# Kernel optimization log

Hardware: AMD Instinct MI355X
Metric: run time of the kernel (lower is better)

## Reference

```python
import jax, jax.numpy as jnp
import numpy as np

FEATURE_DIM = 512
NUM_LABEL = 128
NUM_HEADS = 8
K = 8192
THRES = 0.95


def enqueue(queue, keys, count):
    """FIFO enqueue: queue[count:] = queue[:K-count]; queue[:count] = keys[:count].
    queue: [K, d] (transpose of torch layout), keys: [B, d], count: traced int scalar."""
    Kq = queue.shape[0]
    idx = jnp.arange(Kq)
    shifted = jnp.take(queue, jnp.clip(idx - count, 0, Kq - 1), axis=0)
    new_keys = jnp.take(keys, jnp.clip(idx, 0, keys.shape[0] - 1), axis=0)
    return jnp.where((idx < count)[:, None], new_keys, shifted)


def masked_enqueue(queue, keys, mask):
    # torch boolean indexing keeps original order -> stable sort selected to front
    order = jnp.argsort(~mask, stable=True)
    return enqueue(queue, jnp.take(keys, order, axis=0), jnp.sum(mask))


def forward_cross(x, mem_k, mem_v, Wq, Wk, Wo, bo):
    """Multi-head cross-attention: queries x [N,d], keys mem_k [K,d], values mem_v [K,L].
    Per-head scores on feature_dim; value (label) dim not head-split (L % heads != 0 in
    general), heads averaged; output projection L->L."""
    N, d = x.shape
    dh = d // NUM_HEADS
    q = (x @ Wq).reshape(N, NUM_HEADS, dh)
    k = (mem_k @ Wk).reshape(-1, NUM_HEADS, dh)
    scores = jnp.einsum('nhd,khd->hnk', q, k) * (dh ** -0.5)  # [H,N,K]
    attn = jax.nn.softmax(scores, axis=-1).mean(axis=0)       # [N,K]
    return attn @ mem_v @ Wo + bo                             # [N,L]


def setup_inputs() -> dict:
    key = jax.random.key(0)
    ks = jax.random.split(key, 16)
    N, B_LB = 4096, 1024

    def norm_rows(a):
        return a / jnp.linalg.norm(a, axis=1, keepdims=True)

    inp = {
        'anchor_feat': jax.random.normal(ks[0], (N, FEATURE_DIM), jnp.float32),
        'positive_feat': jax.random.normal(ks[1], (N, FEATURE_DIM), jnp.float32),
        'lb_feat': jax.random.normal(ks[2], (B_LB, FEATURE_DIM), jnp.float32),
        'lb_one_hot': jax.random.uniform(ks[3], (B_LB, NUM_LABEL), jnp.float32),
        'logits_x_lb': jax.random.uniform(ks[4], (B_LB, NUM_LABEL), jnp.float32),
        'logits_x_ulb_1': jax.random.uniform(ks[5], (N, NUM_LABEL), jnp.float32),
        'logits_x_ulb_2': jax.random.uniform(ks[6], (N, NUM_LABEL), jnp.float32),
        # queue buffers: stored [K, d] (= torch queue.T); feat queues L2-normalized at init
        'feat_queue1': norm_rows(jax.random.normal(ks[7], (K, FEATURE_DIM), jnp.float32)),
        'feat_queue2': norm_rows(jax.random.normal(ks[8], (K, FEATURE_DIM), jnp.float32)),
        'label_queue1': norm_rows(jax.random.normal(ks[9], (K, NUM_LABEL), jnp.float32)),
        'label_queue2': norm_rows(jax.random.normal(ks[10], (K, NUM_LABEL), jnp.float32)),
        # Block (cross-attention) parameters
        'Wq': jax.random.normal(ks[11], (FEATURE_DIM, FEATURE_DIM), jnp.float32) * (FEATURE_DIM ** -0.5),
        'Wk': jax.random.normal(ks[12], (FEATURE_DIM, FEATURE_DIM), jnp.float32) * (FEATURE_DIM ** -0.5),
        'Wo': jax.random.normal(ks[13], (NUM_LABEL, NUM_LABEL), jnp.float32) * (NUM_LABEL ** -0.5),
        'bo': jnp.zeros((NUM_LABEL,), jnp.float32),
    }
    return inp


def reference(anchor_feat, positive_feat, lb_feat, lb_one_hot, logits_x_lb,
              logits_x_ulb_1, logits_x_ulb_2,
              feat_queue1, feat_queue2, label_queue1, label_queue2,
              Wq, Wk, Wo, bo):
    sg = jax.lax.stop_gradient  # enqueue is @torch.no_grad()
    B = lb_feat.shape[0] // 2
    lb_feat_1, lb_feat_2 = sg(lb_feat[:B]), sg(lb_feat[B:])
    lb_oh_1, lb_oh_2 = sg(lb_one_hot[:B]), sg(lb_one_hot[B:])

    # queue 1: labeled chunk 1, then high-confidence anchors
    fq1 = enqueue(feat_queue1, lb_feat_1, B)
    lq1 = enqueue(label_queue1, lb_oh_1, B)
    ulb_1_max = jnp.max(logits_x_ulb_1, axis=1) > THRES
    fq1 = masked_enqueue(fq1, sg(anchor_feat), ulb_1_max)
    lq1 = masked_enqueue(lq1, sg(logits_x_ulb_1), ulb_1_max)

    # queue 2: labeled chunk 2, then high-confidence positives
    fq2 = enqueue(feat_queue2, lb_feat_2, B)
    lq2 = enqueue(label_queue2, lb_oh_2, B)
    ulb_2_max = jnp.max(logits_x_ulb_2, axis=1) > THRES
    fq2 = masked_enqueue(fq2, sg(positive_feat), ulb_2_max)
    lq2 = masked_enqueue(lq2, sg(logits_x_ulb_2), ulb_2_max)

    out1 = forward_cross(anchor_feat, fq1, lq1, Wq, Wk, Wo, bo)
    out2 = forward_cross(positive_feat, fq2, lq2, Wq, Wk, Wo, bo)
    # stacked new ulb logits (other original outputs are identity passthroughs)
    return jnp.stack([out1, out2], axis=0)
```

## Files before the change

### kernel.cpp

```cpp
#include <hip/hip_runtime.h>

typedef __bf16 bf16;
typedef __bf16 bf16x8 __attribute__((ext_vector_type(8)));
typedef float f32x4 __attribute__((ext_vector_type(4)));

#define MFMA16(a,b,c) __builtin_amdgcn_mfma_f32_16x16x32_bf16(a,b,c,0,0,0)

#if __has_builtin(__builtin_amdgcn_exp2f)
#define EXP2(x) __builtin_amdgcn_exp2f(x)
#else
#define EXP2(x) exp2f(x)
#endif

#define GLOAD16(g, l) __builtin_amdgcn_global_load_lds( \
    (const __attribute__((address_space(1))) void*)(g), \
    (__attribute__((address_space(3))) void*)(l), 16, 0, 0)

#define N_Q   4096
#define DFEAT 512
#define KQ    8192
#define NLAB  128
#define NHEAD 8
#define KVB   32

#define MBv (1024ull*1024ull)
#define OFF_COUNTS 0ull
#define OFF_MODE   512ull
#define OFF_FLAGS  1024ull
#define OFF_SEL    (64ull*1024ull)
#define OFF_FQ1    (1ull*MBv)
#define OFF_FQ2    (9ull*MBv)
#define OFF_LQ1    (17ull*MBv)
#define OFF_LQ2    (19ull*MBv)
#define OFF_Q1     (21ull*MBv)
#define OFF_Q2     (25ull*MBv)
#define OFF_K1     (29ull*MBv)
#define OFF_WQT    (45ull*MBv)
#define OFF_WKT    (46ull*MBv)
#define OFF_WOT    (47ull*MBv)
#define OFF_VWT    (48ull*MBv)
#define OFF_ACC    (52ull*MBv)

__device__ __forceinline__ float loads(const void* p, size_t i, int f32m) {
    return f32m ? ((const float*)p)[i] : (float)((const bf16*)p)[i];
}
__device__ __forceinline__ bf16x8 load8(const void* p, size_t i, int f32m) {
    bf16x8 r;
    if (f32m) {
        const float4* q = (const float4*)((const float*)p + i);
        float4 f0 = q[0], f1 = q[1];
        r[0] = (bf16)f0.x; r[1] = (bf16)f0.y; r[2] = (bf16)f0.z; r[3] = (bf16)f0.w;
        r[4] = (bf16)f1.x; r[5] = (bf16)f1.y; r[6] = (bf16)f1.z; r[7] = (bf16)f1.w;
    } else {
        r = *(const bf16x8*)((const bf16*)p + i);
    }
    return r;
}

__global__ void detect_kernel(const void* probe, int* mode) {
    const unsigned short* u = (const unsigned short*)probe;
    int t = threadIdx.x;
    int bad = 0;
    for (int i = t; i < 2048; i += 256) {
        unsigned short v = u[2 * i];
        int e = (v >> 7) & 0xFF;
        if (e > 140 || (e < 60 && e != 0)) bad++;
    }
    __shared__ int sb[256];
    sb[t] = bad;
    __syncthreads();
    for (int off = 128; off; off >>= 1) {
        if (t < off) sb[t] += sb[t + off];
        __syncthreads();
    }
    if (t == 0) mode[0] = (sb[0] > 200) ? 1 : 0;
}

__global__ void flag_kernel(const void* __restrict__ ulb1, const void* __restrict__ ulb2,
                            int* __restrict__ flags, const int* __restrict__ modep) {
    int f32m = *modep;
    int row = blockIdx.x, s = blockIdx.y, t = threadIdx.x;
    const void* p = s ? ulb2 : ulb1;
    size_t base = (size_t)row * NLAB;
    float m = fmaxf(loads(p, base + t, f32m), loads(p, base + t + 64, f32m));
    #pragma unroll
    for (int off = 32; off; off >>= 1) m = fmaxf(m, __shfl_xor(m, off));
    if (t == 0) flags[s * N_Q + row] = (m > 0.95f) ? 1 : 0;
}

__global__ void scan_kernel(const int* __restrict__ flags, int* __restrict__ sel,
                            int* __restrict__ counts) {
    int s = blockIdx.x, t = threadIdx.x;
    const int* f = flags + s * N_Q;
    int* selp = sel + s * N_Q;
    __shared__ int ls[1024];
    int f0 = f[t*4], f1 = f[t*4+1], f2 = f[t*4+2], f3 = f[t*4+3];
    int local = f0 + f1 + f2 + f3;
    ls[t] = local;
    __syncthreads();
    for (int off = 1; off < 1024; off <<= 1) {
        int v = (t >= off) ? ls[t - off] : 0;
        __syncthreads();
        ls[t] += v;
        __syncthreads();
    }
    int pos = ls[t] - local;
    if (f0) selp[pos++] = t*4;
    if (f1) selp[pos++] = t*4+1;
    if (f2) selp[pos++] = t*4+2;
    if (f3) selp[pos++] = t*4+3;
    if (t == 1023) counts[s] = ls[1023];
}

__global__ void buildq_kernel(const void* __restrict__ anchor, const void* __restrict__ positive,
                              const void* __restrict__ lbfeat, const void* __restrict__ lboh,
                              const void* __restrict__ ulb1, const void* __restrict__ ulb2,
                              const void* __restrict__ fq1i, const void* __restrict__ fq2i,
                              const void* __restrict__ lq1i, const void* __restrict__ lq2i,
                              const int* __restrict__ sel, const int* __restrict__ counts,
                              bf16* __restrict__ fq1o, bf16* __restrict__ fq2o,
                              bf16* __restrict__ lq1o, bf16* __restrict__ lq2o,
                              const int* __restrict__ modep) {
    int f32m = *modep;
    int i = blockIdx.x, s = blockIdx.y, t = threadIdx.x;
    int C = counts[s];
    const void *fb, *lb;
    size_t frow, lrow;
    if (i < C) {
        int r = sel[s * N_Q + i];
        fb = s ? positive : anchor; frow = r;
        lb = s ? ulb2 : ulb1;       lrow = r;
    } else if (i < C + 512) {
        int r = i - C + s * 512;
        fb = lbfeat; frow = r;
        lb = lboh;   lrow = r;
    } else {
        int r = i - C - 512;
        fb = s ? fq2i : fq1i; frow = r;
        lb = s ? lq2i : lq1i; lrow = r;
    }
    bf16* fd = (s ? fq2o : fq1o) + (size_t)i * DFEAT;
    bf16* ld = (s ? lq2o : lq1o) + (size_t)i * NLAB;
    if (t < 64)      *(bf16x8*)&fd[t * 8]        = load8(fb, frow * DFEAT + (size_t)t * 8, f32m);
    else if (t < 80) *(bf16x8*)&ld[(t - 64) * 8] = load8(lb, lrow * NLAB + (size_t)(t - 64) * 8, f32m);
}

__global__ void transpose_kernel(const void* __restrict__ W, bf16* __restrict__ T, int n,
                                 const int* __restrict__ modep) {
    int f32m = *modep;
    __shared__ bf16 tile[32][33];
    int bx = blockIdx.x * 32, by = blockIdx.y * 32;
    int tx = threadIdx.x & 31, ty = threadIdx.x >> 5;
    for (int r = ty; r < 32; r += 8) tile[r][tx] = (bf16)loads(W, (size_t)(by + r) * n + bx + tx, f32m);
    __syncthreads();
    for (int r = ty; r < 32; r += 8) T[(size_t)(bx + r) * n + by + tx] = tile[tx][r];
}

__launch_bounds__(256, 2)
__global__ void gemm_nt(const void* __restrict__ A, const void* __restrict__ A2,
                        const bf16* __restrict__ B,
                        bf16* __restrict__ C, bf16* __restrict__ C2,
                        int M, int N, int Kd, float alpha,
                        const int* __restrict__ modep, int a_raw, int swz) {
    int f32m = a_raw ? *modep : 0;
    if (blockIdx.z) { A = A2; C = C2; }
    __shared__ __align__(16) bf16 As[128 * 72];
    __shared__ __align__(16) bf16 Bs[128 * 72];
    int m0 = blockIdx.x * 128, n0 = blockIdx.y * 128;
    int t = threadIdx.x, lane = t & 63, wid = t >> 6;
    int quad = lane >> 4, l15 = lane & 15;
    int wrow = (wid >> 1) * 64, wcol = (wid & 1) * 64;
    int srow = t >> 1, sseg = t & 1;
    f32x4 acc[4][4] = {};
    for (int k0 = 0; k0 < Kd; k0 += 32) {
        __syncthreads();
        bf16x8 a0 = load8(A, (size_t)(m0 + srow) * Kd + k0 + sseg * 8, f32m);
        bf16x8 a1 = load8(A, (size_t)(m0 + srow) * Kd + k0 + (sseg + 2) * 8, f32m);
        const uint4* gb = (const uint4*)(B + (size_t)(n0 + srow) * Kd + k0);
        uint4 b0 = gb[sseg], b1 = gb[sseg + 2];
        *(bf16x8*)&As[srow * 72 + sseg * 8]       = a0;
        *(bf16x8*)&As[srow * 72 + (sseg + 2) * 8] = a1;
        *(uint4*)&Bs[srow * 72 + sseg * 8]        = b0;
        *(uint4*)&Bs[srow * 72 + (sseg + 2) * 8]  = b1;
        __syncthreads();
        bf16x8 af[4], bfr[4];
        #pragma unroll
        for (int mt = 0; mt < 4; mt++) af[mt]  = *(const bf16x8*)&As[(wrow + mt*16 + l15) * 72 + quad * 8];
        #pragma unroll
        for (int nt = 0; nt < 4; nt++) bfr[nt] = *(const bf16x8*)&Bs[(wcol + nt*16 + l15) * 72 + quad * 8];
        #pragma unroll
        for (int mt = 0; mt < 4; mt++)
            #pragma unroll
            for (int nt = 0; nt < 4; nt++)
                acc[mt][nt] = MFMA16(af[mt], bfr[nt], acc[mt][nt]);
    }
    #pragma unroll
    for (int mt = 0; mt < 4; mt++)
        #pragma unroll
        for (int nt = 0; nt < 4; nt++)
            #pragma unroll
            for (int r = 0; r < 4; r++) {
                int row = m0 + wrow + mt*16 + quad*4 + r;
                int col = n0 + wcol + nt*16 + l15;
                if (swz) col = (col & ~31) | (((col & 12) << 1) | ((col & 16) >> 2) | (col & 3));
                C[(size_t)row * N + col] = (bf16)(acc[mt][nt][r] * alpha);
            }
}

__launch_bounds__(256, 2)
__global__ void flash3_kernel(const bf16* __restrict__ q1, const bf16* __restrict__ q2,
                              const bf16* __restrict__ kbase, const bf16* __restrict__ vbase,
                              float* __restrict__ acc_out) {
    __shared__ __align__(16) char smem[49152];
    int qb = blockIdx.x, h = blockIdx.y, s = blockIdx.z;
    const bf16* Q  = s ? q2 : q1;
    const bf16* Kp = kbase + (size_t)s * KQ * DFEAT + h * 64;
    const bf16* Vp = vbase + (size_t)s * KQ;
    int t = threadIdx.x, lane = t & 63, wid = t >> 6;
    int quad = lane >> 4, l15 = lane & 15;
    int wq = wid & 1, wh = wid >> 1;
    int qbase = qb * 128 + wq * 64;

    bf16x8 qf[4][2];
    #pragma unroll
    for (int mt = 0; mt < 4; mt++)
        #pragma unroll
        for (int ch = 0; ch < 2; ch++)
            qf[mt][ch] = *(const bf16x8*)(Q + (size_t)(qbase + mt*16 + l15) * DFEAT + h*64 + ch*32 + quad*8);

    bf16x8 onesf;
    #pragma unroll
    for (int i = 0; i < 8; i++) onesf[i] = (bf16)1.0f;

    bf16* Kt = (bf16*)smem;
    bf16* Vt = (bf16*)(smem + 16384);

    int srow8 = lane >> 3;
    int sslot = (lane & 7) ^ srow8;
    const bf16* KgH = Kp + (size_t)(wh * 4096) * DFEAT + (size_t)srow8 * DFEAT + sslot * 8;
    const bf16* VgH = Vp + wh * 4096 + (size_t)(2*srow8 + (sslot >> 2)) * (2 * KQ) + (sslot & 3) * 8;

    const int h7 = l15 & 7;
    int kro[2][2], vro[8];
    #pragma unroll
    for (int nt = 0; nt < 2; nt++)
        #pragma unroll
        for (int ch = 0; ch < 2; ch++)
            kro[nt][ch] = (nt*16 + l15) * 64 + (((ch*4 + quad) ^ h7) << 3);
    #pragma unroll
    for (int ct = 0; ct < 8; ct++)
        vro[ct] = (ct*8 + (l15 >> 1)) * 64 + (((((l15 & 1) << 2) | quad) ^ (l15 >> 1)) << 3);

    {
        bf16* kb = Kt + (size_t)(wh*2 + 0) * 2048;
        bf16* vb = Vt + (size_t)(wh*2 + 0) * 4096;
        if (wq == 0) {
            #pragma unroll
            for (int c = 0; c < 4; c++) GLOAD16(KgH + (size_t)c*8*DFEAT, kb + c*512);
            #pragma unroll
            for (int c = 0; c < 2; c++) GLOAD16(VgH + (size_t)c*16*(2*KQ), vb + c*512);
        } else {
            #pragma unroll
            for (int c = 2; c < 8; c++) GLOAD16(VgH + (size_t)c*16*(2*KQ), vb + c*512);
        }
    }
    __syncthreads();

    f32x4 O[4][8] = {};
    f32x4 L[4] = {};

    for (int it = 0; it < 4096 / KVB; it++) {
        int p = it & 1;
        if (it + 1 < 4096 / KVB) {
            int kvn = (it + 1) * KVB;
            bf16* kb = Kt + (size_t)(wh*2 + (p^1)) * 2048;
            bf16* vb = Vt + (size_t)(wh*2 + (p^1)) * 4096;
            if (wq == 0) {
                #pragma unroll
                for (int c = 0; c < 4; c++) GLOAD16(KgH + (size_t)kvn*DFEAT + (size_t)c*8*DFEAT, kb + c*512);
                #pragma unroll
                for (int c = 0; c < 2; c++) GLOAD16(VgH + kvn + (size_t)c*16*(2*KQ), vb + c*512);
            } else {
                #pragma unroll
                for (int c = 2; c < 8; c++) GLOAD16(VgH + kvn + (size_t)c*16*(2*KQ), vb + c*512);
            }
        }
        const bf16* Kb = Kt + (size_t)(wh*2 + p) * 2048;
        const bf16* Vb = Vt + (size_t)(wh*2 + p) * 4096;

        bf16x8 kf[2][2];
        #pragma unroll
        for (int nt = 0; nt < 2; nt++)
            #pragma unroll
            for (int ch = 0; ch < 2; ch++)
                kf[nt][ch] = *(const bf16x8*)&Kb[kro[nt][ch]];

        bf16x8 P[4];
        __builtin_amdgcn_s_setprio(1);
        #pragma unroll
        for (int mt = 0; mt < 4; mt++) {
            f32x4 s0 = {}, s1 = {};
            s0 = MFMA16(kf[0][0], qf[mt][0], s0);
            s0 = MFMA16(kf[0][1], qf[mt][1], s0);
            s1 = MFMA16(kf[1][0], qf[mt][0], s1);
            s1 = MFMA16(kf[1][1], qf[mt][1], s1);
            bf16x8 pp;
            #pragma unroll
            for (int r = 0; r < 4; r++) {
                pp[r]     = (bf16)EXP2(s0[r]);
                pp[4 + r] = (bf16)EXP2(s1[r]);
            }
            P[mt] = pp;
        }
        #pragma unroll
        for (int mt = 0; mt < 4; mt++) L[mt] = MFMA16(P[mt], onesf, L[mt]);
        #pragma unroll
        for (int ct = 0; ct < 8; ct++) {
            bf16x8 vf = *(const bf16x8*)&Vb[vro[ct]];
            #pragma unroll
            for (int mt = 0; mt < 4; mt++)
                O[mt][ct] = MFMA16(P[mt], vf, O[mt][ct]);
        }
        __builtin_amdgcn_s_setprio(0);
        __syncthreads();
    }

    f32x4* MP = (f32x4*)smem;
    int midx = lane * 36;
    #pragma unroll
    for (int pass = 0; pass < 2; pass++) {
        if (wh == 1 && wq == pass) {
            #pragma unroll
            for (int mt = 0; mt < 4; mt++) {
                #pragma unroll
                for (int ct = 0; ct < 8; ct++) MP[midx + mt*8 + ct] = O[mt][ct];
                MP[midx + 32 + mt] = L[mt];
            }
        }
        __syncthreads();
        if (wh == 0 && wq == pass) {
            #pragma unroll
            for (int mt = 0; mt < 4; mt++) {
                f32x4 lp = MP[midx + 32 + mt];
                float invr[4];
                #pragma unroll
                for (int r = 0; r < 4; r++) invr[r] = 1.0f / (8.0f * (L[mt][r] + lp[r]));
                #pragma unroll
                for (int ct = 0; ct < 8; ct++) {
                    f32x4 op = MP[midx + mt*8 + ct];
                    #pragma unroll
                    for (int r = 0; r < 4; r++) {
                        int row = qbase + mt*16 + quad*4 + r;
                        atomicAdd(&acc_out[((size_t)s * N_Q + row) * NLAB + ct*16 + l15],
                                  (O[mt][ct][r] + op[r]) * invr[r]);
                    }
                }
            }
        }
        __syncthreads();
    }
}

__global__ void bias_kernel(const float* __restrict__ acc, const void* __restrict__ bo,
                            void* __restrict__ out, const int* __restrict__ modep) {
    int f32m = *modep;
    int idx = blockIdx.x * 256 + threadIdx.x;
    float v = acc[idx] + loads(bo, idx & (NLAB - 1), f32m);
    if (f32m) ((float*)out)[idx] = v;
    else      ((bf16*)out)[idx] = (bf16)v;
}

extern "C" void kernel_launch(void* const* d_in, const int* in_sizes, int n_in,
                              void* d_out, int out_size, void* d_ws, size_t ws_size,
                              hipStream_t stream) {
    const void* anchor   = d_in[0];
    const void* positive = d_in[1];
    const void* lbfeat   = d_in[2];
    const void* lboh     = d_in[3];
    const void* ulb1     = d_in[5];
    const void* ulb2     = d_in[6];
    const void* fq1i     = d_in[7];
    const void* fq2i     = d_in[8];
    const void* lq1i     = d_in[9];
    const void* lq2i     = d_in[10];
    const void* Wq       = d_in[11];
    const void* Wk       = d_in[12];
    const void* Wo       = d_in[13];
    const void* bo       = d_in[14];

    char* ws = (char*)d_ws;
    int*  counts = (int*)(ws + OFF_COUNTS);
    int*  modep  = (int*)(ws + OFF_MODE);
    int*  flags  = (int*)(ws + OFF_FLAGS);
    int*  sel    = (int*)(ws + OFF_SEL);
    bf16* fq1  = (bf16*)(ws + OFF_FQ1);
    bf16* fq2  = (bf16*)(ws + OFF_FQ2);
    bf16* lq1  = (bf16*)(ws + OFF_LQ1);
    bf16* lq2  = (bf16*)(ws + OFF_LQ2);
    bf16* q1   = (bf16*)(ws + OFF_Q1);
    bf16* q2   = (bf16*)(ws + OFF_Q2);
    bf16* k1   = (bf16*)(ws + OFF_K1);
    bf16* wqT  = (bf16*)(ws + OFF_WQT);
    bf16* wkT  = (bf16*)(ws + OFF_WKT);
    bf16* woT  = (bf16*)(ws + OFF_WOT);
    bf16* vwt  = (bf16*)(ws + OFF_VWT);
    float* accb = (float*)(ws + OFF_ACC);

    hipMemsetAsync(accb, 0, (size_t)2 * N_Q * NLAB * sizeof(float), stream);

    detect_kernel<<<1, 256, 0, stream>>>(anchor, modep);
    flag_kernel<<<dim3(N_Q, 2), 64, 0, stream>>>(ulb1, ulb2, flags, modep);
    scan_kernel<<<2, 1024, 0, stream>>>(flags, sel, counts);
    buildq_kernel<<<dim3(KQ, 2), 128, 0, stream>>>(anchor, positive, lbfeat, lboh, ulb1, ulb2,
                                                   fq1i, fq2i, lq1i, lq2i, sel, counts,
                                                   fq1, fq2, lq1, lq2, modep);
    transpose_kernel<<<dim3(16, 16), 256, 0, stream>>>(Wq, wqT, 512, modep);
    transpose_kernel<<<dim3(16, 16), 256, 0, stream>>>(Wk, wkT, 512, modep);
    transpose_kernel<<<dim3(4, 4), 256, 0, stream>>>(Wo, woT, 128, modep);

    const float qalpha = 0.125f * 1.44269504088896f;
    gemm_nt<<<dim3(32, 4, 2), 256, 0, stream>>>(anchor, positive, wqT, q1, q2,
                                                4096, 512, 512, qalpha, modep, 1, 0);
    gemm_nt<<<dim3(128, 4, 1), 256, 0, stream>>>(fq1, nullptr, wkT, k1, nullptr,
                                                 16384, 512, 512, 1.0f, modep, 0, 0);
    gemm_nt<<<dim3(1, 128, 1), 256, 0, stream>>>(woT, nullptr, lq1, vwt, nullptr,
                                                 128, 16384, 128, 1.0f, modep, 0, 0);

    flash3_kernel<<<dim3(32, NHEAD, 2), 256, 0, stream>>>(q1, q2, k1, vwt, accb);
    bias_kernel<<<(2 * N_Q * NLAB) / 256, 256, 0, stream>>>(accb, bo, d_out, modep);
}
```

Measured before the change: 372.1 us.

## Merge setup and projection kernels into fewer launches with inline dtype probe

Replaces the separate detect, flag and three transpose kernels with one prep kernel, and the three projection GEMM launches with a single gemm3 kernel dispatched by block index. Each kernel now works out the input dtype itself from a small probe of the anchor tensor, so there is no longer a mode word in the workspace to read. This cuts the launch count and the serial dependency gaps between small kernels. The smaller probe sample (32 values instead of 2048) could misclassify the dtype on unusual inputs.

```diff
diff --git a/kernel.cpp b/kernel.cpp
--- a/kernel.cpp
+++ b/kernel.cpp
@@ -25,7 +25,6 @@
 
 #define MBv (1024ull*1024ull)
 #define OFF_COUNTS 0ull
-#define OFF_MODE   512ull
 #define OFF_FLAGS  1024ull
 #define OFF_SEL    (64ull*1024ull)
 #define OFF_FQ1    (1ull*MBv)
@@ -41,6 +40,18 @@
 #define OFF_VWT    (48ull*MBv)
 #define OFF_ACC    (52ull*MBv)
 
+__device__ __forceinline__ int probe_f32(const void* p) {
+    const unsigned short* u = (const unsigned short*)p;
+    int bad = 0;
+    #pragma unroll
+    for (int i = 0; i < 32; i++) {
+        unsigned short v = u[2 * i];
+        int e = (v >> 7) & 0xFF;
+        if (e > 140 || (e < 60 && e != 0)) bad++;
+    }
+    return bad > 3;
+}
+
 __device__ __forceinline__ float loads(const void* p, size_t i, int f32m) {
     return f32m ? ((const float*)p)[i] : (float)((const bf16*)p)[i];
 }
@@ -57,35 +68,43 @@
     return r;
 }
 
-__global__ void detect_kernel(const void* probe, int* mode) {
-    const unsigned short* u = (const unsigned short*)probe;
-    int t = threadIdx.x;
-    int bad = 0;
-    for (int i = t; i < 2048; i += 256) {
-        unsigned short v = u[2 * i];
-        int e = (v >> 7) & 0xFF;
-        if (e > 140 || (e < 60 && e != 0)) bad++;
-    }
-    __shared__ int sb[256];
-    sb[t] = bad;
+__device__ __forceinline__ void do_transpose(const void* W, bf16* T, int n,
+                                             int bxi, int byi, int f32m, bf16 (*tile)[33]) {
+    int bx = bxi * 32, by = byi * 32;
+    int tx = threadIdx.x & 31, ty = threadIdx.x >> 5;
+    for (int r = ty; r < 32; r += 8) tile[r][tx] = (bf16)loads(W, (size_t)(by + r) * n + bx + tx, f32m);
     __syncthreads();
-    for (int off = 128; off; off >>= 1) {
-        if (t < off) sb[t] += sb[t + off];
-        __syncthreads();
-    }
-    if (t == 0) mode[0] = (sb[0] > 200) ? 1 : 0;
-}
-
-__global__ void flag_kernel(const void* __restrict__ ulb1, const void* __restrict__ ulb2,
-                            int* __restrict__ flags, const int* __restrict__ modep) {
-    int f32m = *modep;
-    int row = blockIdx.x, s = blockIdx.y, t = threadIdx.x;
-    const void* p = s ? ulb2 : ulb1;
-    size_t base = (size_t)row * NLAB;
-    float m = fmaxf(loads(p, base + t, f32m), loads(p, base + t + 64, f32m));
-    #pragma unroll
-    for (int off = 32; off; off >>= 1) m = fmaxf(m, __shfl_xor(m, off));
-    if (t == 0) flags[s * N_Q + row] = (m > 0.95f) ? 1 : 0;
+    for (int r = ty; r < 32; r += 8) T[(size_t)(bx + r) * n + by + tx] = tile[tx][r];
+}
+
+__global__ void prep_kernel(const void* __restrict__ Wq, const void* __restrict__ Wk,
+                            const void* __restrict__ Wo,
+                            bf16* __restrict__ wqT, bf16* __restrict__ wkT, bf16* __restrict__ woT,
+                            const void* __restrict__ ulb1, const void* __restrict__ ulb2,
+                            int* __restrict__ flags, const void* __restrict__ probe) {
+    __shared__ bf16 tile[32][33];
+    int f32m = probe_f32(probe);
+    int b = blockIdx.x, t = threadIdx.x;
+    if (b < 2048) {
+        int idx = b * 4 + (t >> 6);
+        int lane = t & 63;
+        int s = idx >> 12, row = idx & 4095;
+        const void* p = s ? ulb2 : ulb1;
+        size_t base = (size_t)row * NLAB;
+        float m = fmaxf(loads(p, base + lane, f32m), loads(p, base + lane + 64, f32m));
+        #pragma unroll
+        for (int off = 32; off; off >>= 1) m = fmaxf(m, __shfl_xor(m, off));
+        if (lane == 0) flags[s * N_Q + row] = (m > 0.95f) ? 1 : 0;
+    } else if (b < 2304) {
+        int tb = b - 2048;
+        do_transpose(Wq, wqT, 512, tb & 15, tb >> 4, f32m, tile);
+    } else if (b < 2560) {
+        int tb = b - 2304;
+        do_transpose(Wk, wkT, 512, tb & 15, tb >> 4, f32m, tile);
+    } else {
+        int tb = b - 2560;
+        do_transpose(Wo, woT, 128, tb & 3, tb >> 2, f32m, tile);
+    }
 }
 
 __global__ void scan_kernel(const int* __restrict__ flags, int* __restrict__ sel,
@@ -120,8 +139,8 @@
                               const int* __restrict__ sel, const int* __restrict__ counts,
                               bf16* __restrict__ fq1o, bf16* __restrict__ fq2o,
                               bf16* __restrict__ lq1o, bf16* __restrict__ lq2o,
-                              const int* __restrict__ modep) {
-    int f32m = *modep;
+                              const void* __restrict__ probe) {
+    int f32m = probe_f32(probe);
     int i = blockIdx.x, s = blockIdx.y, t = threadIdx.x;
     int C = counts[s];
     const void *fb, *lb;
@@ -145,28 +164,10 @@
     else if (t < 80) *(bf16x8*)&ld[(t - 64) * 8] = load8(lb, lrow * NLAB + (size_t)(t - 64) * 8, f32m);
 }
 
-__global__ void transpose_kernel(const void* __restrict__ W, bf16* __restrict__ T, int n,
-                                 const int* __restrict__ modep) {
-    int f32m = *modep;
-    __shared__ bf16 tile[32][33];
-    int bx = blockIdx.x * 32, by = blockIdx.y * 32;
-    int tx = threadIdx.x & 31, ty = threadIdx.x >> 5;
-    for (int r = ty; r < 32; r += 8) tile[r][tx] = (bf16)loads(W, (size_t)(by + r) * n + bx + tx, f32m);
-    __syncthreads();
-    for (int r = ty; r < 32; r += 8) T[(size_t)(bx + r) * n + by + tx] = tile[tx][r];
-}
-
-__launch_bounds__(256, 2)
-__global__ void gemm_nt(const void* __restrict__ A, const void* __restrict__ A2,
-                        const bf16* __restrict__ B,
-                        bf16* __restrict__ C, bf16* __restrict__ C2,
-                        int M, int N, int Kd, float alpha,
-                        const int* __restrict__ modep, int a_raw, int swz) {
-    int f32m = a_raw ? *modep : 0;
-    if (blockIdx.z) { A = A2; C = C2; }
-    __shared__ __align__(16) bf16 As[128 * 72];
-    __shared__ __align__(16) bf16 Bs[128 * 72];
-    int m0 = blockIdx.x * 128, n0 = blockIdx.y * 128;
+__device__ __forceinline__ void gemm_body(const void* __restrict__ A, const bf16* __restrict__ B,
+                                          bf16* __restrict__ C, int N, int Kd, float alpha,
+                                          int f32m, int m0, int n0,
+                                          bf16* As, bf16* Bs) {
     int t = threadIdx.x, lane = t & 63, wid = t >> 6;
     int quad = lane >> 4, l15 = lane & 15;
     int wrow = (wid >> 1) * 64, wcol = (wid & 1) * 64;
@@ -202,9 +203,33 @@
             for (int r = 0; r < 4; r++) {
                 int row = m0 + wrow + mt*16 + quad*4 + r;
                 int col = n0 + wcol + nt*16 + l15;
-                if (swz) col = (col & ~31) | (((col & 12) << 1) | ((col & 16) >> 2) | (col & 3));
                 C[(size_t)row * N + col] = (bf16)(acc[mt][nt][r] * alpha);
             }
+}
+
+__launch_bounds__(256, 2)
+__global__ void gemm3_kernel(const void* __restrict__ anchor, const void* __restrict__ positive,
+                             const bf16* __restrict__ fq1, const bf16* __restrict__ woT,
+                             const bf16* __restrict__ lq1,
+                             const bf16* __restrict__ wqT, const bf16* __restrict__ wkT,
+                             bf16* __restrict__ q1, bf16* __restrict__ q2,
+                             bf16* __restrict__ k1, bf16* __restrict__ vwt,
+                             const void* __restrict__ probe) {
+    __shared__ __align__(16) bf16 As[128 * 72];
+    __shared__ __align__(16) bf16 Bs[128 * 72];
+    int b = blockIdx.x;
+    if (b < 256) {
+        int f32m = probe_f32(probe);
+        int s = b >> 7, r = b & 127;
+        gemm_body(s ? positive : anchor, wqT, s ? q2 : q1, 512, 512,
+                  0.125f * 1.44269504088896f, f32m, (r >> 2) * 128, (r & 3) * 128, As, Bs);
+    } else if (b < 768) {
+        int r = b - 256;
+        gemm_body(fq1, wkT, k1, 512, 512, 1.0f, 0, (r >> 2) * 128, (r & 3) * 128, As, Bs);
+    } else {
+        int r = b - 768;
+        gemm_body(woT, lq1, vwt, 16384, 128, 1.0f, 0, 0, r * 128, As, Bs);
+    }
 }
 
 __launch_bounds__(256, 2)
@@ -362,8 +387,8 @@
 }
 
 __global__ void bias_kernel(const float* __restrict__ acc, const void* __restrict__ bo,
-                            void* __restrict__ out, const int* __restrict__ modep) {
-    int f32m = *modep;
+                            void* __restrict__ out, const void* __restrict__ probe) {
+    int f32m = probe_f32(probe);
     int idx = blockIdx.x * 256 + threadIdx.x;
     float v = acc[idx] + loads(bo, idx & (NLAB - 1), f32m);
     if (f32m) ((float*)out)[idx] = v;
@@ -390,7 +415,6 @@
 
     char* ws = (char*)d_ws;
     int*  counts = (int*)(ws + OFF_COUNTS);
-    int*  modep  = (int*)(ws + OFF_MODE);
     int*  flags  = (int*)(ws + OFF_FLAGS);
     int*  sel    = (int*)(ws + OFF_SEL);
     bf16* fq1  = (bf16*)(ws + OFF_FQ1);
@@ -408,24 +432,15 @@
 
     hipMemsetAsync(accb, 0, (size_t)2 * N_Q * NLAB * sizeof(float), stream);
 
-    detect_kernel<<<1, 256, 0, stream>>>(anchor, modep);
-    flag_kernel<<<dim3(N_Q, 2), 64, 0, stream>>>(ulb1, ulb2, flags, modep);
+    prep_kernel<<<2576, 256, 0, stream>>>(Wq, Wk, Wo, wqT, wkT, woT,
+                                          ulb1, ulb2, flags, anchor);
     scan_kernel<<<2, 1024, 0, stream>>>(flags, sel, counts);
     buildq_kernel<<<dim3(KQ, 2), 128, 0, stream>>>(anchor, positive, lbfeat, lboh, ulb1, ulb2,
                                                    fq1i, fq2i, lq1i, lq2i, sel, counts,
-                                                   fq1, fq2, lq1, lq2, modep);
-    transpose_kernel<<<dim3(16, 16), 256, 0, stream>>>(Wq, wqT, 512, modep);
-    transpose_kernel<<<dim3(16, 16), 256, 0, stream>>>(Wk, wkT, 512, modep);
-    transpose_kernel<<<dim3(4, 4), 256, 0, stream>>>(Wo, woT, 128, modep);
-
-    const float qalpha = 0.125f * 1.44269504088896f;
-    gemm_nt<<<dim3(32, 4, 2), 256, 0, stream>>>(anchor, positive, wqT, q1, q2,
-                                                4096, 512, 512, qalpha, modep, 1, 0);
-    gemm_nt<<<dim3(128, 4, 1), 256, 0, stream>>>(fq1, nullptr, wkT, k1, nullptr,
-                                                 16384, 512, 512, 1.0f, modep, 0, 0);
-    gemm_nt<<<dim3(1, 128, 1), 256, 0, stream>>>(woT, nullptr, lq1, vwt, nullptr,
-                                                 128, 16384, 128, 1.0f, modep, 0, 0);
+                                                   fq1, fq2, lq1, lq2, anchor);
+    gemm3_kernel<<<896, 256, 0, stream>>>(anchor, positive, fq1, woT, lq1, wqT, wkT,
+                                          q1, q2, k1, vwt, anchor);
 
     flash3_kernel<<<dim3(32, NHEAD, 2), 256, 0, stream>>>(q1, q2, k1, vwt, accb);
-    bias_kernel<<<(2 * N_Q * NLAB) / 256, 256, 0, stream>>>(accb, bo, d_out, modep);
-}
+    bias_kernel<<<(2 * N_Q * NLAB) / 256, 256, 0, stream>>>(accb, bo, d_out, anchor);
+}
```

Result: faster. 357.6 us (-3.9%).
